# Optimization experiments

Measured on AMD Instinct MI355X. Metric: run time of the kernel, lower is better.

The kernel has to match this reference:

```python
import jax, jax.numpy as jnp
import numpy as np

B, L, S = 8192, 1024, 3
OUTSIDE, TM_HELIX, INSIDE = 0, 1, 2


def setup_inputs() -> dict:
    key = jax.random.key(0)
    k1, k2 = jax.random.split(key)
    emissions = jax.random.normal(k1, (B, L, S), dtype=jnp.float32)
    tags = jax.random.randint(k2, (B, L), 0, S)
    mask = jnp.ones((B, L), dtype=jnp.float32)
    t = np.zeros((S, S), dtype=np.float32)
    t[OUTSIDE, INSIDE] = -5.0
    t[INSIDE, OUTSIDE] = -5.0
    t[OUTSIDE, TM_HELIX] = 1.0
    t[INSIDE, TM_HELIX] = 1.0
    t[TM_HELIX, OUTSIDE] = 1.0
    t[TM_HELIX, INSIDE] = 1.0
    transitions = jnp.asarray(t)
    return {"emissions": emissions, "mask": mask, "transitions": transitions, "tags": tags}


def _score_sentence(emissions, tags, mask, transitions):
    # emission score of the gold tag at every position: (B, L)
    em_score = jnp.take_along_axis(emissions, tags[..., None], axis=2)[..., 0]
    # transition score between consecutive gold tags: (B, L-1)
    trans_score = transitions[tags[:, :-1], tags[:, 1:]]
    return em_score[:, 0] * mask[:, 0] + jnp.sum(
        (trans_score + em_score[:, 1:]) * mask[:, 1:], axis=1
    )


def _forward_alg(emissions, mask, transitions):
    def step(alpha, xs):
        em_t, m_t = xs  # (B, S), (B,)
        # scores[b, i, j] = alpha[b, i] + T[i, j] + em_t[b, j]
        scores = alpha[:, :, None] + transitions[None, :, :] + em_t[:, None, :]
        new_alpha = jax.nn.logsumexp(scores, axis=1)
        alpha = jnp.where(m_t[:, None] > 0, new_alpha, alpha)
        return alpha, None

    alpha0 = emissions[:, 0, :]
    xs = (jnp.swapaxes(emissions[:, 1:, :], 0, 1),  # (L-1, B, S)
          jnp.swapaxes(mask[:, 1:], 0, 1))          # (L-1, B)
    alpha, _ = jax.lax.scan(step, alpha0, xs)
    return jax.nn.logsumexp(alpha, axis=1)  # (B,)


def reference(emissions, mask, transitions, tags):
    logZ = _forward_alg(emissions, mask, transitions)
    gold = _score_sentence(emissions, tags, mask, transitions)
    return jnp.mean(logZ - gold)
```

## Files before the change

### kernel.cpp

```cpp
#include <hip/hip_runtime.h>


#define LOG2E 1.4426950408889634f
#define LN2   0.6931471805599453f

constexpr int B = 8192;
constexpr int W = 4;
constexpr int LSTRIDE = 14;

__device__ __forceinline__ float fexp2(float x) { return __builtin_amdgcn_exp2f(x); }
__device__ __forceinline__ float flog2(float x) { return __builtin_amdgcn_logf(x); }

__device__ __forceinline__ float mux3(float a, float b, float c, int i) {
  return i == 0 ? a : (i == 1 ? b : c);
}
__device__ __forceinline__ float trmux(const float* __restrict__ T2, int p, int c) {
  const float r0 = mux3(T2[0], T2[1], T2[2], c);
  const float r1 = mux3(T2[3], T2[4], T2[5], c);
  const float r2 = mux3(T2[6], T2[7], T2[8], c);
  return mux3(r0, r1, r2, p);
}

__device__ __forceinline__ void matmul3(float* __restrict__ D,
                                        const float* __restrict__ A,
                                        const float* __restrict__ Bm) {
  #pragma unroll
  for (int i = 0; i < 3; ++i)
    #pragma unroll
    for (int j = 0; j < 3; ++j)
      D[i * 3 + j] = A[i * 3 + 0] * Bm[0 * 3 + j] +
                     A[i * 3 + 1] * Bm[1 * 3 + j] +
                     A[i * 3 + 2] * Bm[2 * 3 + j];
}

__device__ __forceinline__ void renorm3(float* __restrict__ P, float& scale) {
  float m = P[0];
  #pragma unroll
  for (int e = 1; e < 9; ++e) m = fmaxf(m, P[e]);
  int ex;
  (void)frexpf(m, &ex);
  #pragma unroll
  for (int e = 0; e < 9; ++e) P[e] = ldexpf(P[e], -ex);
  scale += (float)ex;
}

__global__ __launch_bounds__(256, 4) void crf_main(
    const float* __restrict__ em, const float* __restrict__ mask,
    const float* __restrict__ trans, const int* __restrict__ tags,
    float* __restrict__ out) {
  __shared__ __align__(16) float s_em[W][64 * LSTRIDE];
  __shared__ float red[W];

  const int lane = threadIdx.x & 63;
  const int wid  = threadIdx.x >> 6;
  const int b    = blockIdx.x * W + wid;
  float* lds = s_em[wid];

  const float4* em4 = (const float4*)(em + (size_t)b * 3072);
  const float4* mk4 = (const float4*)(mask + (size_t)b * 1024);
  const int4*   tg4 = (const int4*)(tags + (size_t)b * 1024);

  float4 em_r[2][3]; float4 mk_r[2]; int4 tg_r[2];
  #pragma unroll
  for (int u = 0; u < 3; ++u) em_r[0][u] = em4[u * 64 + lane];
  mk_r[0] = mk4[lane];
  tg_r[0] = tg4[lane];
  #pragma unroll
  for (int u = 0; u < 3; ++u) em_r[1][u] = em4[192 + u * 64 + lane];
  mk_r[1] = mk4[64 + lane];
  tg_r[1] = tg4[64 + lane];

  float T2[9], tk[9];
  #pragma unroll
  for (int e = 0; e < 9; ++e) { T2[e] = trans[e] * LOG2E; tk[e] = fexp2(T2[e]); }

  float Pacc[9];
  float scale = 0.f, gold = 0.f;
  float a0 = 0.f, a1 = 0.f, a2 = 0.f;
  int boundaryTag = 0;

  #pragma unroll
  for (int q = 0; q < 4; ++q) {
    const int buf = q & 1;

    #pragma unroll
    for (int u = 0; u < 3; ++u) {
      const float4 v = em_r[buf][u];
      const int t  = u + lane;
      const int l0 = 21 * u + t / 3;
      const int r0 = 4 * (t % 3);
      float2* wp = (float2*)&lds[l0 * LSTRIDE + r0];
      wp[0] = make_float2(v.x, v.y);
      wp[1] = make_float2(v.z, v.w);
    }

    const float mf[4] = {mk_r[buf].x, mk_r[buf].y, mk_r[buf].z, mk_r[buf].w};
    const int   tf[4] = {tg_r[buf].x, tg_r[buf].y, tg_r[buf].z, tg_r[buf].w};

    float P[9];
    float e0sel = 0.f, mk0 = 0.f;
    int tag0 = 0, prev = 0;
    const float2* rp = (const float2*)&lds[lane * LSTRIDE];

    #pragma unroll
    for (int h = 0; h < 2; ++h) {
      float eb[6];
      #pragma unroll
      for (int r = 0; r < 3; ++r) {
        const float2 t = rp[3 * h + r];
        eb[2 * r] = t.x; eb[2 * r + 1] = t.y;
      }
      #pragma unroll
      for (int jj = 0; jj < 2; ++jj) {
        const int j = 2 * h + jj;
        const float ev0 = eb[3 * jj + 0] * LOG2E;
        const float ev1 = eb[3 * jj + 1] * LOG2E;
        const float ev2 = eb[3 * jj + 2] * LOG2E;
        const float m = mf[j];
        const int cur = tf[j];

        const float e = mux3(ev0, ev1, ev2, cur);
        if (j == 0) { e0sel = e; mk0 = m; tag0 = cur; }
        else        gold = fmaf(trmux(T2, prev, cur) + e, m, gold);
        prev = cur;

        const float w0 = fexp2(ev0), w1 = fexp2(ev1), w2 = fexp2(ev2);
        if (q == 0 && j == 0) { a0 = w0; a1 = w1; a2 = w2; }
        const bool act = (m > 0.f) && !(q == 0 && j == 0 && lane == 0);
        const float g = act ? 1.f : 0.f;
        const float c1 = 1.f - g;
        const float u0 = w0 * g, u1 = w1 * g, u2 = w2 * g;
        float M[9];
        M[0] = fmaf(tk[0], u0, c1); M[1] = tk[1] * u1;          M[2] = tk[2] * u2;
        M[3] = tk[3] * u0;          M[4] = fmaf(tk[4], u1, c1); M[5] = tk[5] * u2;
        M[6] = tk[6] * u0;          M[7] = tk[7] * u1;          M[8] = fmaf(tk[8], u2, c1);
        if (j == 0) {
          #pragma unroll
          for (int e2 = 0; e2 < 9; ++e2) P[e2] = M[e2];
        } else {
          float N[9];
          matmul3(N, P, M);
          #pragma unroll
          for (int e2 = 0; e2 < 9; ++e2) P[e2] = N[e2];
        }
      }
    }

    const int prevLast = __shfl_up(prev, 1, 64);
    const int bt = (lane == 0) ? boundaryTag : prevLast;
    const float tr0 = trmux(T2, bt, tag0);
    const float tplus = (q == 0 && lane == 0) ? 0.f : tr0;
    gold = fmaf(tplus + e0sel, mk0, gold);
    boundaryTag = __shfl(prev, 63, 64);

    float sc = 0.f;
    renorm3(P, sc);
    #pragma unroll
    for (int d = 1; d < 64; d <<= 1) {
      float o[9];
      #pragma unroll
      for (int e2 = 0; e2 < 9; ++e2) o[e2] = __shfl_xor(P[e2], d, 64);
      const float osc = __shfl_xor(sc, d, 64);
      const bool later = (lane & d) != 0;
      float A[9], Bm[9];
      #pragma unroll
      for (int e2 = 0; e2 < 9; ++e2) {
        A[e2]  = later ? o[e2] : P[e2];
        Bm[e2] = later ? P[e2] : o[e2];
      }
      float N[9];
      matmul3(N, A, Bm);
      #pragma unroll
      for (int e2 = 0; e2 < 9; ++e2) P[e2] = N[e2];
      sc += osc;
    }
    scale += sc;

    if (q == 0) {
      #pragma unroll
      for (int e2 = 0; e2 < 9; ++e2) Pacc[e2] = P[e2];
    } else {
      float N[9];
      matmul3(N, Pacc, P);
      #pragma unroll
      for (int e2 = 0; e2 < 9; ++e2) Pacc[e2] = N[e2];
    }

    if (q < 2) {
      #pragma unroll
      for (int u = 0; u < 3; ++u) em_r[buf][u] = em4[(q + 2) * 192 + u * 64 + lane];
      mk_r[buf] = mk4[(q + 2) * 64 + lane];
      tg_r[buf] = tg4[(q + 2) * 64 + lane];
    }
  }

  #pragma unroll
  for (int d = 1; d < 64; d <<= 1) gold += __shfl_xor(gold, d, 64);

  if (lane == 0) {
    const float z = a0 * (Pacc[0] + Pacc[1] + Pacc[2]) +
                    a1 * (Pacc[3] + Pacc[4] + Pacc[5]) +
                    a2 * (Pacc[6] + Pacc[7] + Pacc[8]);
    red[wid] = LN2 * (scale + flog2(z) - gold);
  }
  __syncthreads();
  if (threadIdx.x == 0) {
    const float s = red[0] + red[1] + red[2] + red[3];
    atomicAdd(out, s * (1.0f / (float)B));
  }
}

extern "C" void kernel_launch(void* const* d_in, const int* in_sizes, int n_in,
                              void* d_out, int out_size, void* d_ws, size_t ws_size,
                              hipStream_t stream) {
  const float* em    = (const float*)d_in[0];
  const float* mask  = (const float*)d_in[1];
  const float* trans = (const float*)d_in[2];
  const int*   tags  = (const int*)d_in[3];
  float* out = (float*)d_out;

  hipMemsetAsync(out, 0, sizeof(float), stream);
  crf_main<<<B / W, 256, 0, stream>>>(em, mask, trans, tags, out);
}
```

Baseline: 227.1 us.

## Process sequence in two 512-step halves with LDS-staged mask/tags and scan-up prefix

Splits each sequence into two halves of 512 positions, so each lane handles 8 consecutive steps instead of 4 per quarter. Emissions are pre-scaled by log2e and staged in LDS together with mask and tags, with tags packed as bytes. The butterfly xor all-reduce of 3x3 matrix products becomes an inclusive shfl_up scan, and the final product is read from lane 63. This halves the number of cross-lane reductions and the per-quarter overhead, at the cost of more registers and LDS per lane, which may affect occupancy.

Result: faster. 216.7 us (-4.6%).

```diff
diff --git a/kernel.cpp b/kernel.cpp
--- a/kernel.cpp
+++ b/kernel.cpp
@@ -6,7 +6,9 @@
 
 constexpr int B = 8192;
 constexpr int W = 4;
-constexpr int LSTRIDE = 14;
+constexpr int EM_ST = 25;
+constexpr int MK_ST = 9;
+constexpr int TG_ST = 3;
 
 __device__ __forceinline__ float fexp2(float x) { return __builtin_amdgcn_exp2f(x); }
 __device__ __forceinline__ float flog2(float x) { return __builtin_amdgcn_logf(x); }
@@ -44,164 +46,175 @@
   scale += (float)ex;
 }
 
+__device__ __forceinline__ void scat_em(float* __restrict__ L, int lane, int u, float4 v) {
+  const int K = 64 * u + lane;
+  const int a = EM_ST * (K / 6) + 4 * (K % 6);
+  L[a + 0] = v.x * LOG2E; L[a + 1] = v.y * LOG2E;
+  L[a + 2] = v.z * LOG2E; L[a + 3] = v.w * LOG2E;
+}
+__device__ __forceinline__ void scat_mk(float* __restrict__ L, int lane, int u, float4 v) {
+  const int K = 64 * u + lane;
+  const int a = MK_ST * (K >> 1) + 4 * (K & 1);
+  L[a + 0] = v.x; L[a + 1] = v.y; L[a + 2] = v.z; L[a + 3] = v.w;
+}
+__device__ __forceinline__ void scat_tg(unsigned* __restrict__ L, int lane, int u, int4 t) {
+  const int K = 64 * u + lane;
+  const unsigned pk = (unsigned)(t.x & 3) | ((unsigned)(t.y & 3) << 8) |
+                      ((unsigned)(t.z & 3) << 16) | ((unsigned)(t.w & 3) << 24);
+  L[TG_ST * (K >> 1) + (K & 1)] = pk;
+}
+
+template <int H>
+__device__ __forceinline__ void compute_half(
+    const float* __restrict__ Lem, const float* __restrict__ Lmk,
+    const unsigned* __restrict__ Ltg, int lane,
+    const float* __restrict__ T2, const float* __restrict__ tk,
+    float* __restrict__ Pout, float& scOut,
+    float& gold, int& boundaryTag, float& a0, float& a1, float& a2) {
+  const float* eml = Lem + EM_ST * lane;
+  const float* mkl = Lmk + MK_ST * lane;
+  const unsigned pk0 = Ltg[TG_ST * lane + 0];
+  const unsigned pk1 = Ltg[TG_ST * lane + 1];
+
+  float P[9];
+  float e0sel = 0.f, mk0 = 0.f;
+  int tag0 = 0, prev = 0;
+
+  #pragma unroll
+  for (int j = 0; j < 8; ++j) {
+    const float ev0 = eml[3 * j + 0];
+    const float ev1 = eml[3 * j + 1];
+    const float ev2 = eml[3 * j + 2];
+    const float m = mkl[j];
+    const int cur = (int)(((j < 4 ? pk0 : pk1) >> (8 * (j & 3))) & 3u);
+
+    const float e = mux3(ev0, ev1, ev2, cur);
+    if (j == 0) { e0sel = e; mk0 = m; tag0 = cur; }
+    else        gold = fmaf(trmux(T2, prev, cur) + e, m, gold);
+    prev = cur;
+
+    const float w0 = fexp2(ev0), w1 = fexp2(ev1), w2 = fexp2(ev2);
+    if (H == 0 && j == 0) { a0 = w0; a1 = w1; a2 = w2; }
+    const bool act = (m > 0.f) && !(H == 0 && j == 0 && lane == 0);
+    const float g = act ? 1.f : 0.f;
+    const float c1 = 1.f - g;
+    const float u0 = w0 * g, u1 = w1 * g, u2 = w2 * g;
+    float M[9];
+    M[0] = fmaf(tk[0], u0, c1); M[1] = tk[1] * u1;          M[2] = tk[2] * u2;
+    M[3] = tk[3] * u0;          M[4] = fmaf(tk[4], u1, c1); M[5] = tk[5] * u2;
+    M[6] = tk[6] * u0;          M[7] = tk[7] * u1;          M[8] = fmaf(tk[8], u2, c1);
+    if (j == 0) {
+      #pragma unroll
+      for (int e2 = 0; e2 < 9; ++e2) P[e2] = M[e2];
+    } else {
+      float N[9];
+      matmul3(N, P, M);
+      #pragma unroll
+      for (int e2 = 0; e2 < 9; ++e2) P[e2] = N[e2];
+    }
+  }
+
+  const int prevLast = __shfl_up(prev, 1, 64);
+  const int bt = (lane == 0) ? boundaryTag : prevLast;
+  const float tr0 = trmux(T2, bt, tag0);
+  const float tplus = (H == 0 && lane == 0) ? 0.f : tr0;
+  gold = fmaf(tplus + e0sel, mk0, gold);
+  boundaryTag = __shfl(prev, 63, 64);
+
+  float sc = 0.f;
+  renorm3(P, sc);
+
+  #pragma unroll
+  for (int d = 1; d < 64; d <<= 1) {
+    float o0 = __shfl_up(P[0], d, 64), o1 = __shfl_up(P[1], d, 64);
+    float o2 = __shfl_up(P[2], d, 64), o3 = __shfl_up(P[3], d, 64);
+    float o4 = __shfl_up(P[4], d, 64), o5 = __shfl_up(P[5], d, 64);
+    float o6 = __shfl_up(P[6], d, 64), o7 = __shfl_up(P[7], d, 64);
+    float o8 = __shfl_up(P[8], d, 64);
+    float osc = __shfl_up(sc, d, 64);
+    const bool in = (lane >= d);
+    float O[9];
+    O[0] = in ? o0 : 1.f; O[1] = in ? o1 : 0.f; O[2] = in ? o2 : 0.f;
+    O[3] = in ? o3 : 0.f; O[4] = in ? o4 : 1.f; O[5] = in ? o5 : 0.f;
+    O[6] = in ? o6 : 0.f; O[7] = in ? o7 : 0.f; O[8] = in ? o8 : 1.f;
+    float N[9];
+    matmul3(N, O, P);
+    #pragma unroll
+    for (int e2 = 0; e2 < 9; ++e2) P[e2] = N[e2];
+    sc += in ? osc : 0.f;
+  }
+  #pragma unroll
+  for (int e2 = 0; e2 < 9; ++e2) Pout[e2] = P[e2];
+  scOut = sc;
+}
+
 __global__ __launch_bounds__(256, 4) void crf_main(
     const float* __restrict__ em, const float* __restrict__ mask,
     const float* __restrict__ trans, const int* __restrict__ tags,
     float* __restrict__ out) {
-  __shared__ __align__(16) float s_em[W][64 * LSTRIDE];
+  __shared__ float    s_em[W][64 * EM_ST];
+  __shared__ float    s_mk[W][64 * MK_ST];
+  __shared__ unsigned s_tg[W][64 * TG_ST];
   __shared__ float red[W];
 
   const int lane = threadIdx.x & 63;
   const int wid  = threadIdx.x >> 6;
   const int b    = blockIdx.x * W + wid;
-  float* lds = s_em[wid];
+  float*    Lem = s_em[wid];
+  float*    Lmk = s_mk[wid];
+  unsigned* Ltg = s_tg[wid];
 
   const float4* em4 = (const float4*)(em + (size_t)b * 3072);
   const float4* mk4 = (const float4*)(mask + (size_t)b * 1024);
   const int4*   tg4 = (const int4*)(tags + (size_t)b * 1024);
 
-  float4 em_r[2][3]; float4 mk_r[2]; int4 tg_r[2];
-  #pragma unroll
-  for (int u = 0; u < 3; ++u) em_r[0][u] = em4[u * 64 + lane];
-  mk_r[0] = mk4[lane];
-  tg_r[0] = tg4[lane];
-  #pragma unroll
-  for (int u = 0; u < 3; ++u) em_r[1][u] = em4[192 + u * 64 + lane];
-  mk_r[1] = mk4[64 + lane];
-  tg_r[1] = tg4[64 + lane];
+  const float4 e0 = em4[lane],        e1 = em4[64 + lane],  e2 = em4[128 + lane];
+  const float4 e3 = em4[192 + lane],  e4 = em4[256 + lane], e5 = em4[320 + lane];
+  const float4 m0 = mk4[lane],        m1 = mk4[64 + lane];
+  const int4   t0 = tg4[lane],        t1 = tg4[64 + lane];
 
   float T2[9], tk[9];
   #pragma unroll
   for (int e = 0; e < 9; ++e) { T2[e] = trans[e] * LOG2E; tk[e] = fexp2(T2[e]); }
 
-  float Pacc[9];
-  float scale = 0.f, gold = 0.f;
+  scat_em(Lem, lane, 0, e0); scat_em(Lem, lane, 1, e1); scat_em(Lem, lane, 2, e2);
+  scat_em(Lem, lane, 3, e3); scat_em(Lem, lane, 4, e4); scat_em(Lem, lane, 5, e5);
+  scat_mk(Lmk, lane, 0, m0); scat_mk(Lmk, lane, 1, m1);
+  scat_tg(Ltg, lane, 0, t0); scat_tg(Ltg, lane, 1, t1);
+
+  const float4 f0 = em4[384 + lane], f1 = em4[448 + lane], f2 = em4[512 + lane];
+  const float4 f3 = em4[576 + lane], f4v = em4[640 + lane], f5 = em4[704 + lane];
+  const float4 n0 = mk4[128 + lane], n1 = mk4[192 + lane];
+  const int4   s0 = tg4[128 + lane], s1 = tg4[192 + lane];
+
+  float gold = 0.f;
+  int boundaryTag = 0;
   float a0 = 0.f, a1 = 0.f, a2 = 0.f;
-  int boundaryTag = 0;
-
-  #pragma unroll
-  for (int q = 0; q < 4; ++q) {
-    const int buf = q & 1;
-
-    #pragma unroll
-    for (int u = 0; u < 3; ++u) {
-      const float4 v = em_r[buf][u];
-      const int t  = u + lane;
-      const int l0 = 21 * u + t / 3;
-      const int r0 = 4 * (t % 3);
-      float2* wp = (float2*)&lds[l0 * LSTRIDE + r0];
-      wp[0] = make_float2(v.x, v.y);
-      wp[1] = make_float2(v.z, v.w);
-    }
-
-    const float mf[4] = {mk_r[buf].x, mk_r[buf].y, mk_r[buf].z, mk_r[buf].w};
-    const int   tf[4] = {tg_r[buf].x, tg_r[buf].y, tg_r[buf].z, tg_r[buf].w};
-
-    float P[9];
-    float e0sel = 0.f, mk0 = 0.f;
-    int tag0 = 0, prev = 0;
-    const float2* rp = (const float2*)&lds[lane * LSTRIDE];
-
-    #pragma unroll
-    for (int h = 0; h < 2; ++h) {
-      float eb[6];
-      #pragma unroll
-      for (int r = 0; r < 3; ++r) {
-        const float2 t = rp[3 * h + r];
-        eb[2 * r] = t.x; eb[2 * r + 1] = t.y;
-      }
-      #pragma unroll
-      for (int jj = 0; jj < 2; ++jj) {
-        const int j = 2 * h + jj;
-        const float ev0 = eb[3 * jj + 0] * LOG2E;
-        const float ev1 = eb[3 * jj + 1] * LOG2E;
-        const float ev2 = eb[3 * jj + 2] * LOG2E;
-        const float m = mf[j];
-        const int cur = tf[j];
-
-        const float e = mux3(ev0, ev1, ev2, cur);
-        if (j == 0) { e0sel = e; mk0 = m; tag0 = cur; }
-        else        gold = fmaf(trmux(T2, prev, cur) + e, m, gold);
-        prev = cur;
-
-        const float w0 = fexp2(ev0), w1 = fexp2(ev1), w2 = fexp2(ev2);
-        if (q == 0 && j == 0) { a0 = w0; a1 = w1; a2 = w2; }
-        const bool act = (m > 0.f) && !(q == 0 && j == 0 && lane == 0);
-        const float g = act ? 1.f : 0.f;
-        const float c1 = 1.f - g;
-        const float u0 = w0 * g, u1 = w1 * g, u2 = w2 * g;
-        float M[9];
-        M[0] = fmaf(tk[0], u0, c1); M[1] = tk[1] * u1;          M[2] = tk[2] * u2;
-        M[3] = tk[3] * u0;          M[4] = fmaf(tk[4], u1, c1); M[5] = tk[5] * u2;
-        M[6] = tk[6] * u0;          M[7] = tk[7] * u1;          M[8] = fmaf(tk[8], u2, c1);
-        if (j == 0) {
-          #pragma unroll
-          for (int e2 = 0; e2 < 9; ++e2) P[e2] = M[e2];
-        } else {
-          float N[9];
-          matmul3(N, P, M);
-          #pragma unroll
-          for (int e2 = 0; e2 < 9; ++e2) P[e2] = N[e2];
-        }
-      }
-    }
-
-    const int prevLast = __shfl_up(prev, 1, 64);
-    const int bt = (lane == 0) ? boundaryTag : prevLast;
-    const float tr0 = trmux(T2, bt, tag0);
-    const float tplus = (q == 0 && lane == 0) ? 0.f : tr0;
-    gold = fmaf(tplus + e0sel, mk0, gold);
-    boundaryTag = __shfl(prev, 63, 64);
-
-    float sc = 0.f;
-    renorm3(P, sc);
-    #pragma unroll
-    for (int d = 1; d < 64; d <<= 1) {
-      float o[9];
-      #pragma unroll
-      for (int e2 = 0; e2 < 9; ++e2) o[e2] = __shfl_xor(P[e2], d, 64);
-      const float osc = __shfl_xor(sc, d, 64);
-      const bool later = (lane & d) != 0;
-      float A[9], Bm[9];
-      #pragma unroll
-      for (int e2 = 0; e2 < 9; ++e2) {
-        A[e2]  = later ? o[e2] : P[e2];
-        Bm[e2] = later ? P[e2] : o[e2];
-      }
-      float N[9];
-      matmul3(N, A, Bm);
-      #pragma unroll
-      for (int e2 = 0; e2 < 9; ++e2) P[e2] = N[e2];
-      sc += osc;
-    }
-    scale += sc;
-
-    if (q == 0) {
-      #pragma unroll
-      for (int e2 = 0; e2 < 9; ++e2) Pacc[e2] = P[e2];
-    } else {
-      float N[9];
-      matmul3(N, Pacc, P);
-      #pragma unroll
-      for (int e2 = 0; e2 < 9; ++e2) Pacc[e2] = N[e2];
-    }
-
-    if (q < 2) {
-      #pragma unroll
-      for (int u = 0; u < 3; ++u) em_r[buf][u] = em4[(q + 2) * 192 + u * 64 + lane];
-      mk_r[buf] = mk4[(q + 2) * 64 + lane];
-      tg_r[buf] = tg4[(q + 2) * 64 + lane];
-    }
-  }
+  float PA[9], PB[9];
+  float scA, scB;
+
+  compute_half<0>(Lem, Lmk, Ltg, lane, T2, tk, PA, scA, gold, boundaryTag, a0, a1, a2);
+
+  scat_em(Lem, lane, 0, f0); scat_em(Lem, lane, 1, f1); scat_em(Lem, lane, 2, f2);
+  scat_em(Lem, lane, 3, f3); scat_em(Lem, lane, 4, f4v); scat_em(Lem, lane, 5, f5);
+  scat_mk(Lmk, lane, 0, n0); scat_mk(Lmk, lane, 1, n1);
+  scat_tg(Ltg, lane, 0, s0); scat_tg(Ltg, lane, 1, s1);
+
+  compute_half<1>(Lem, Lmk, Ltg, lane, T2, tk, PB, scB, gold, boundaryTag, a0, a1, a2);
 
   #pragma unroll
   for (int d = 1; d < 64; d <<= 1) gold += __shfl_xor(gold, d, 64);
-
-  if (lane == 0) {
-    const float z = a0 * (Pacc[0] + Pacc[1] + Pacc[2]) +
-                    a1 * (Pacc[3] + Pacc[4] + Pacc[5]) +
-                    a2 * (Pacc[6] + Pacc[7] + Pacc[8]);
-    red[wid] = LN2 * (scale + flog2(z) - gold);
+  const float af0 = __shfl(a0, 0, 64);
+  const float af1 = __shfl(a1, 0, 64);
+  const float af2 = __shfl(a2, 0, 64);
+
+  if (lane == 63) {
+    float Pt[9];
+    matmul3(Pt, PA, PB);
+    const float z = af0 * (Pt[0] + Pt[1] + Pt[2]) +
+                    af1 * (Pt[3] + Pt[4] + Pt[5]) +
+                    af2 * (Pt[6] + Pt[7] + Pt[8]);
+    red[wid] = LN2 * (scA + scB + flog2(z) - gold);
   }
   __syncthreads();
   if (threadIdx.x == 0) {
```
